# Kernel tuning notes

Measured on AMD Instinct MI355X. Metric: run time of the kernel, lower is better.

## Reference

```python
import jax, jax.numpy as jnp
import numpy as np

EMBED = 256
NUM_DEPTH = 128
NUM_CAMS = 1


def _bilinear_sample(img, x, y):
    # img: [H, W, E]; x, y: [L] pixel coords (align_corners=False, zero padding)
    H, W, _ = img.shape
    x0f = jnp.floor(x); y0f = jnp.floor(y)
    ix0 = x0f.astype(jnp.int32); iy0 = y0f.astype(jnp.int32)
    ix1 = ix0 + 1; iy1 = iy0 + 1
    wx1 = x - x0f; wx0 = 1.0 - wx1
    wy1 = y - y0f; wy0 = 1.0 - wy1

    def g(iy, ix):
        valid = (ix >= 0) & (ix < W) & (iy >= 0) & (iy < H)
        v = img[jnp.clip(iy, 0, H - 1), jnp.clip(ix, 0, W - 1)]  # [L, E]
        return jnp.where(valid[:, None], v, jnp.zeros((), img.dtype))

    return (g(iy0, ix0) * (wy0 * wx0)[:, None] + g(iy0, ix1) * (wy0 * wx1)[:, None]
            + g(iy1, ix0) * (wy1 * wx0)[:, None] + g(iy1, ix1) * (wy1 * wx1)[:, None])


def setup_inputs() -> dict:
    rng = jax.random.key(0)
    ks = jax.random.split(rng, 7)
    H = W = 64
    nv = H * W           # num_value == num_query (forced by output*key broadcast)
    bsv = 1
    return {
        "query": jax.random.normal(ks[0], (bsv, nv, EMBED), jnp.float32),
        "key": jax.random.normal(ks[1], (NUM_CAMS, nv, bsv, EMBED), jnp.float32),
        "value": jax.random.normal(ks[2], (NUM_CAMS, nv, bsv, EMBED), jnp.float32),
        "identity": jax.random.normal(ks[3], (bsv, nv, NUM_DEPTH), jnp.float32),
        "ref_3d": jax.random.uniform(ks[4], (bsv * NUM_CAMS, nv * NUM_DEPTH, 2), jnp.float32),
        "spatial_shapes": jnp.array([[H, W]], jnp.int32),
        "W_attn": jax.random.normal(ks[5], (NUM_CAMS * NUM_DEPTH, EMBED), jnp.float32) * 0.02,
        "b_attn": jax.random.normal(ks[6], (NUM_CAMS * NUM_DEPTH,), jnp.float32) * 0.02,
    }


def reference(query, key, value, identity, ref_3d, spatial_shapes, W_attn, b_attn):
    bsv, num_query, _ = query.shape
    num_cams, num_value, bs, _ = key.shape
    H = int(spatial_shapes[0, 0]); W = int(spatial_shapes[0, 1])

    # key/value rearrange (value flipped over cams dim, a no-op for num_cams=1)
    key_r = jnp.transpose(key, (2, 0, 1, 3)).reshape(bsv, num_value, EMBED)
    val_r = jnp.transpose(value[::-1], (2, 0, 1, 3)).reshape(bsv * num_cams, num_value, EMBED)

    # attention weights: Linear -> softmax over (levels*points)=1 axis (== ones)
    aw = query @ W_attn.T + b_attn                               # [bsv, nq, cams*depth]
    aw = aw.reshape(bsv, num_query, num_cams, NUM_DEPTH, 1, 1)    # heads=1, lv*pt=1
    aw = jax.nn.softmax(aw, axis=-1)
    aw = jnp.transpose(aw.reshape(bsv, num_query, num_cams, NUM_DEPTH, 1, 1, 1),
                       (0, 2, 1, 3, 4, 5, 6))
    aw = aw.reshape(bsv * num_cams, num_query * NUM_DEPTH)        # [B, L]

    # deformable bilinear sampling (single level/head/point)
    grids = 2.0 * ref_3d - 1.0                                   # grid_sample convention
    px = ((grids[..., 0] + 1.0) * W - 1.0) / 2.0                  # [B, L]
    py = ((grids[..., 1] + 1.0) * H - 1.0) / 2.0
    imgs = val_r.reshape(bsv * num_cams, H, W, EMBED)
    sampled = jax.vmap(_bilinear_sample)(imgs, px, py)            # [B, L, E]

    out = sampled * aw[:, :, None]                                # weighted gather
    out = out.reshape(bsv, num_cams, num_query, NUM_DEPTH, EMBED).mean(axis=1)

    # elementwise dot with key features, scaled
    out = jnp.sum(out * key_r[:, :, None, :], axis=-1) / jnp.sqrt(jnp.float32(EMBED))
    return out + identity                                         # [bsv, nq, num_depth]
```

## Files before the change

### kernel.cpp

```cpp
#include <hip/hip_runtime.h>

#define EMBED 256
#define NUM_DEPTH 128
#define CT_STRIDE 136

typedef __attribute__((ext_vector_type(8))) short bf16x8;
typedef __attribute__((ext_vector_type(4))) float f32x4;

__device__ __forceinline__ unsigned short f2b(float f) {
    union { float f; unsigned u; } c; c.f = f;
    unsigned u = c.u;
    u += 0x7fffu + ((u >> 16) & 1u);
    return (unsigned short)(u >> 16);
}
__device__ __forceinline__ float b2f(unsigned short h) {
    union { unsigned u; float f; } c; c.u = ((unsigned)h) << 16;
    return c.f;
}

__global__ __launch_bounds__(256) void cvt_kernel(
    const float4* __restrict__ key, const float4* __restrict__ val,
    ushort4* __restrict__ kb, ushort4* __restrict__ vb, int n4)
{
    int i = blockIdx.x * blockDim.x + threadIdx.x;
    if (i >= n4) return;
    float4 a = key[i];
    float4 b = val[i];
    kb[i] = make_ushort4(f2b(a.x), f2b(a.y), f2b(a.z), f2b(a.w));
    vb[i] = make_ushort4(f2b(b.x), f2b(b.y), f2b(b.z), f2b(b.w));
}

__global__ __launch_bounds__(256) void gemm_nt_bf16(
    const unsigned short* __restrict__ A,
    const unsigned short* __restrict__ B,
    unsigned short* __restrict__ D,
    int N)
{
    __shared__ __align__(16) unsigned short Ct[128 * CT_STRIDE];
    unsigned short* As = Ct;
    unsigned short* Bs = Ct + 128 * 32;

    const int m0 = blockIdx.y * 128;
    const int n0 = blockIdx.x * 128;
    const int tid  = threadIdx.x;
    const int lane = tid & 63;
    const int wave = tid >> 6;
    const int wm = (wave & 1) * 64;
    const int wn = (wave >> 1) * 64;

    f32x4 acc[4][4] = {};

    const int srow = lane >> 2;
    const int scol = (lane & 3) * 8;
    const int k8 = (lane >> 4) * 8;
    const int fm = lane & 15;

    for (int kt = 0; kt < EMBED; kt += 32) {
        #pragma unroll
        for (int t = 0; t < 2; ++t) {
            const int c = wave * 2 + t;
            const int row = c * 16 + srow;
            const unsigned short* ga = A + (size_t)(m0 + row) * EMBED + kt + scol;
            const unsigned short* gb = B + (size_t)(n0 + row) * EMBED + kt + scol;
            __builtin_amdgcn_global_load_lds(
                (const __attribute__((address_space(1))) void*)ga,
                (__attribute__((address_space(3))) void*)(As + c * 512), 16, 0, 0);
            __builtin_amdgcn_global_load_lds(
                (const __attribute__((address_space(1))) void*)gb,
                (__attribute__((address_space(3))) void*)(Bs + c * 512), 16, 0, 0);
        }
        __syncthreads();

        bf16x8 af[4], bfr[4];
        #pragma unroll
        for (int i = 0; i < 4; ++i) {
            af[i]  = *(const bf16x8*)(As + (wm + i * 16 + fm) * 32 + k8);
            bfr[i] = *(const bf16x8*)(Bs + (wn + i * 16 + fm) * 32 + k8);
        }
        #pragma unroll
        for (int i = 0; i < 4; ++i)
            #pragma unroll
            for (int j = 0; j < 4; ++j)
                acc[i][j] = __builtin_amdgcn_mfma_f32_16x16x32_bf16(af[i], bfr[j], acc[i][j], 0, 0, 0);
        __syncthreads();
    }

    const int col = lane & 15;
    const int rbase = (lane >> 4) * 4;
    #pragma unroll
    for (int i = 0; i < 4; ++i)
        #pragma unroll
        for (int j = 0; j < 4; ++j) {
            const int rr = wm + i * 16 + rbase;
            const int cc = wn + j * 16 + col;
            #pragma unroll
            for (int r = 0; r < 4; ++r)
                Ct[(rr + r) * CT_STRIDE + cc] = f2b(acc[i][j][r]);
        }
    __syncthreads();

    #pragma unroll
    for (int it = 0; it < 8; ++it) {
        const int r  = it * 16 + (tid >> 4);
        const int c8 = (tid & 15) * 8;
        const int4 v = *(const int4*)(Ct + r * CT_STRIDE + c8);
        *(int4*)(D + (size_t)(m0 + r) * N + n0 + c8) = v;
    }
}

__global__ __launch_bounds__(256) void gather_kernel(
    const unsigned short* __restrict__ D,
    const float* __restrict__ identity,
    const float* __restrict__ ref3d,
    const int*   __restrict__ spatial,
    float* __restrict__ out, int nv)
{
    __shared__ unsigned short Ds[2 * 4096];

    const int q0 = blockIdx.x * 2;
    const int tid = threadIdx.x;

    const int4* src = (const int4*)(D + (size_t)q0 * nv);
    int4* dst = (int4*)Ds;
    const int nchunk = (2 * nv) / 8;
    for (int i = tid; i < nchunk; i += 256) dst[i] = src[i];
    __syncthreads();

    const int Hs = spatial[0], Ws = spatial[1];
    const int l = q0 * NUM_DEPTH + tid;
    const int qi = tid >> 7;

    const float2 r2 = reinterpret_cast<const float2*>(ref3d)[l];
    const float px = r2.x * (float)Ws - 0.5f;
    const float py = r2.y * (float)Hs - 0.5f;
    const float x0f = floorf(px), y0f = floorf(py);
    const int ix0 = (int)x0f, iy0 = (int)y0f;
    const int ix1 = ix0 + 1,  iy1 = iy0 + 1;
    const float wx1 = px - x0f, wx0 = 1.0f - wx1;
    const float wy1 = py - y0f, wy0 = 1.0f - wy1;
    const bool vx0 = (ix0 >= 0) & (ix0 < Ws);
    const bool vx1 = (ix1 >= 0) & (ix1 < Ws);

    const unsigned short* row = Ds + qi * nv;
    float acc = 0.f;
    if (iy0 >= 0 && iy0 < Hs) {
        if (vx0) acc = fmaf(wy0 * wx0, b2f(row[iy0 * Ws + ix0]), acc);
        if (vx1) acc = fmaf(wy0 * wx1, b2f(row[iy0 * Ws + ix1]), acc);
    }
    if (iy1 >= 0 && iy1 < Hs) {
        if (vx0) acc = fmaf(wy1 * wx0, b2f(row[iy1 * Ws + ix0]), acc);
        if (vx1) acc = fmaf(wy1 * wx1, b2f(row[iy1 * Ws + ix1]), acc);
    }
    out[l] = fmaf(acc, 0.0625f, identity[l]);
}

__global__ __launch_bounds__(256) void uv_direct_kernel(
    const float* __restrict__ key, const float* __restrict__ value,
    const float* __restrict__ identity, const float* __restrict__ ref3d,
    const int* __restrict__ spatial, float* __restrict__ out)
{
    const int q = blockIdx.x;
    const int tid = threadIdx.x;
    const int lane = tid & 63;
    const int wave = tid >> 6;
    const int H = spatial[0], W = spatial[1];
    const int row4 = EMBED / 4;
    const float4 k4 = reinterpret_cast<const float4*>(key + (size_t)q * EMBED)[lane];
    const float4* __restrict__ v4 = reinterpret_cast<const float4*>(value);
    for (int d = wave; d < NUM_DEPTH; d += 4) {
        const int l = q * NUM_DEPTH + d;
        const float rx = ref3d[2 * l], ry = ref3d[2 * l + 1];
        const float px = rx * (float)W - 0.5f, py = ry * (float)H - 0.5f;
        const float x0f = floorf(px), y0f = floorf(py);
        const int ix0 = (int)x0f, iy0 = (int)y0f, ix1 = ix0 + 1, iy1 = iy0 + 1;
        const float wx1 = px - x0f, wx0 = 1.f - wx1, wy1 = py - y0f, wy0 = 1.f - wy1;
        float4 acc = make_float4(0.f, 0.f, 0.f, 0.f);
        #define TAP(IY, IX, WGT) \
            if ((IY) >= 0 && (IY) < H && (IX) >= 0 && (IX) < W) { \
                const float w_ = (WGT); \
                const float4 t = v4[(size_t)((IY) * W + (IX)) * row4 + lane]; \
                acc.x = fmaf(w_, t.x, acc.x); acc.y = fmaf(w_, t.y, acc.y); \
                acc.z = fmaf(w_, t.z, acc.z); acc.w = fmaf(w_, t.w, acc.w); }
        TAP(iy0, ix0, wy0 * wx0) TAP(iy0, ix1, wy0 * wx1)
        TAP(iy1, ix0, wy1 * wx0) TAP(iy1, ix1, wy1 * wx1)
        #undef TAP
        float partial = acc.x * k4.x + acc.y * k4.y + acc.z * k4.z + acc.w * k4.w;
        #pragma unroll
        for (int off = 32; off > 0; off >>= 1) partial += __shfl_xor(partial, off, 64);
        if (lane == 0) out[l] = fmaf(partial, 0.0625f, identity[l]);
    }
}

extern "C" void kernel_launch(void* const* d_in, const int* in_sizes, int n_in,
                              void* d_out, int out_size, void* d_ws, size_t ws_size,
                              hipStream_t stream) {
    const float* key      = (const float*)d_in[1];
    const float* value    = (const float*)d_in[2];
    const float* identity = (const float*)d_in[3];
    const float* ref3d    = (const float*)d_in[4];
    const int*   spatial  = (const int*)d_in[5];
    float* out = (float*)d_out;

    const int nq = in_sizes[3] / NUM_DEPTH;
    const int nv = in_sizes[1] / EMBED;

    const size_t d_bytes  = (size_t)nq * nv * sizeof(unsigned short);
    const size_t kb_bytes = (size_t)nq * EMBED * sizeof(unsigned short);
    const size_t vb_bytes = (size_t)nv * EMBED * sizeof(unsigned short);
    const size_t need = d_bytes + kb_bytes + vb_bytes;

    if (ws_size < need || (nq % 128) || (nv % 128) || nv > 4096 || (nq % 2)) {
        uv_direct_kernel<<<nq, 256, 0, stream>>>(key, value, identity, ref3d, spatial, out);
        return;
    }

    unsigned short* D  = (unsigned short*)d_ws;
    unsigned short* kb = (unsigned short*)((char*)d_ws + d_bytes);
    unsigned short* vb = (unsigned short*)((char*)d_ws + d_bytes + kb_bytes);

    const int n4 = nq * EMBED / 4;
    cvt_kernel<<<(n4 + 255) / 256, 256, 0, stream>>>(
        (const float4*)key, (const float4*)value, (ushort4*)kb, (ushort4*)vb, n4);

    dim3 grid(nv / 128, nq / 128);
    gemm_nt_bf16<<<grid, 256, 0, stream>>>(kb, vb, D, nv);

    gather_kernel<<<nq / 2, 256, 0, stream>>>(D, identity, ref3d, spatial, out, nv);
}
```

Before: 99.56 us.

## Fuse bilinear gather into GEMM epilogue via pre-binned tap lists and atomics

A prep kernel now converts key/value to bf16 and, in the same launch, initialises the output with identity. It also bins every bilinear tap by the value-pixel tile it reads, writing per-(query tile, pixel tile, block) counts and entry lists. The GEMM epilogue then reads each tile's entry list and atomically adds the weighted, scaled dot-product values straight from shared memory into the output. This removes the full nq×nv bf16 intermediate, its write and re-read, and the separate gather launch. In exchange it adds atomics, a workspace for entry lists, and a fixed per-segment capacity that would drop taps if a bin overflows.

```diff
diff --git a/kernel.cpp b/kernel.cpp
--- a/kernel.cpp
+++ b/kernel.cpp
@@ -3,6 +3,8 @@
 #define EMBED 256
 #define NUM_DEPTH 128
 #define CT_STRIDE 136
+#define SEG 128
+#define BPQ 64
 
 typedef __attribute__((ext_vector_type(8))) short bf16x8;
 typedef __attribute__((ext_vector_type(4))) float f32x4;
@@ -18,23 +20,74 @@
     return c.f;
 }
 
-__global__ __launch_bounds__(256) void cvt_kernel(
+__global__ __launch_bounds__(256) void prep_kernel(
     const float4* __restrict__ key, const float4* __restrict__ val,
-    ushort4* __restrict__ kb, ushort4* __restrict__ vb, int n4)
+    ushort4* __restrict__ kb, ushort4* __restrict__ vb, int n4, int cvtBlocks,
+    const float* __restrict__ identity, const float* __restrict__ ref3d,
+    const int* __restrict__ spatial, float* __restrict__ out,
+    unsigned* __restrict__ cnts, unsigned* __restrict__ gent, int NB, int nv)
 {
-    int i = blockIdx.x * blockDim.x + threadIdx.x;
-    if (i >= n4) return;
-    float4 a = key[i];
-    float4 b = val[i];
-    kb[i] = make_ushort4(f2b(a.x), f2b(a.y), f2b(a.z), f2b(a.w));
-    vb[i] = make_ushort4(f2b(b.x), f2b(b.y), f2b(b.z), f2b(b.w));
-}
-
-__global__ __launch_bounds__(256) void gemm_nt_bf16(
+    const int tid = threadIdx.x;
+    if ((int)blockIdx.x < cvtBlocks) {
+        int i = blockIdx.x * 256 + tid;
+        if (i < n4) {
+            float4 a = key[i];
+            float4 b = val[i];
+            kb[i] = make_ushort4(f2b(a.x), f2b(a.y), f2b(a.z), f2b(a.w));
+            vb[i] = make_ushort4(f2b(b.x), f2b(b.y), f2b(b.z), f2b(b.w));
+        }
+        return;
+    }
+
+    __shared__ unsigned cnt[32];
+    if (tid < 32) cnt[tid] = 0;
+    __syncthreads();
+
+    const int bb = blockIdx.x - cvtBlocks;
+    const int l  = bb * 256 + tid;
+    out[l] = identity[l];
+
+    const int Hs = spatial[0], Ws = spatial[1];
+    const float2 r2 = reinterpret_cast<const float2*>(ref3d)[l];
+    const float px = r2.x * (float)Ws - 0.5f;
+    const float py = r2.y * (float)Hs - 0.5f;
+    const float x0f = floorf(px), y0f = floorf(py);
+    const int ix0 = (int)x0f, iy0 = (int)y0f;
+
+    int pbt[4]; unsigned slot[4];
+    #pragma unroll
+    for (int t = 0; t < 4; ++t) {
+        const int ix = ix0 + (t & 1);
+        const int iy = iy0 + (t >> 1);
+        pbt[t] = -1;
+        if (ix >= 0 && ix < Ws && iy >= 0 && iy < Hs) {
+            const int p = iy * Ws + ix;
+            if (p < nv) {
+                pbt[t]  = p >> 7;
+                slot[t] = atomicAdd(&cnt[pbt[t]], 1u);
+            }
+        }
+    }
+    __syncthreads();
+
+    const int qb  = bb >> 6;
+    const int blk = bb & 63;
+    if (tid < NB) cnts[((size_t)qb * NB + tid) * BPQ + blk] = cnt[tid];
+
+    #pragma unroll
+    for (int t = 0; t < 4; ++t)
+        if (pbt[t] >= 0 && slot[t] < SEG)
+            gent[(((size_t)qb * NB + pbt[t]) * BPQ + blk) * SEG + slot[t]] =
+                ((unsigned)l << 2) | (unsigned)t;
+}
+
+__global__ __launch_bounds__(256) void gemm_scatter(
     const unsigned short* __restrict__ A,
     const unsigned short* __restrict__ B,
-    unsigned short* __restrict__ D,
-    int N)
+    const float* __restrict__ ref3d,
+    const int* __restrict__ spatial,
+    float* __restrict__ out,
+    const unsigned* __restrict__ cnts, const unsigned* __restrict__ gent, int NB)
 {
     __shared__ __align__(16) unsigned short Ct[128 * CT_STRIDE];
     unsigned short* As = Ct;
@@ -99,59 +152,30 @@
         }
     __syncthreads();
 
-    #pragma unroll
-    for (int it = 0; it < 8; ++it) {
-        const int r  = it * 16 + (tid >> 4);
-        const int c8 = (tid & 15) * 8;
-        const int4 v = *(const int4*)(Ct + r * CT_STRIDE + c8);
-        *(int4*)(D + (size_t)(m0 + r) * N + n0 + c8) = v;
-    }
-}
-
-__global__ __launch_bounds__(256) void gather_kernel(
-    const unsigned short* __restrict__ D,
-    const float* __restrict__ identity,
-    const float* __restrict__ ref3d,
-    const int*   __restrict__ spatial,
-    float* __restrict__ out, int nv)
-{
-    __shared__ unsigned short Ds[2 * 4096];
-
-    const int q0 = blockIdx.x * 2;
-    const int tid = threadIdx.x;
-
-    const int4* src = (const int4*)(D + (size_t)q0 * nv);
-    int4* dst = (int4*)Ds;
-    const int nchunk = (2 * nv) / 8;
-    for (int i = tid; i < nchunk; i += 256) dst[i] = src[i];
-    __syncthreads();
-
+    const size_t bin = (size_t)blockIdx.y * NB + blockIdx.x;
+    const unsigned* __restrict__ cseg = cnts + bin * BPQ;
+    const unsigned* __restrict__ eseg = gent + bin * BPQ * SEG;
     const int Hs = spatial[0], Ws = spatial[1];
-    const int l = q0 * NUM_DEPTH + tid;
-    const int qi = tid >> 7;
-
-    const float2 r2 = reinterpret_cast<const float2*>(ref3d)[l];
-    const float px = r2.x * (float)Ws - 0.5f;
-    const float py = r2.y * (float)Hs - 0.5f;
-    const float x0f = floorf(px), y0f = floorf(py);
-    const int ix0 = (int)x0f, iy0 = (int)y0f;
-    const int ix1 = ix0 + 1,  iy1 = iy0 + 1;
-    const float wx1 = px - x0f, wx0 = 1.0f - wx1;
-    const float wy1 = py - y0f, wy0 = 1.0f - wy1;
-    const bool vx0 = (ix0 >= 0) & (ix0 < Ws);
-    const bool vx1 = (ix1 >= 0) & (ix1 < Ws);
-
-    const unsigned short* row = Ds + qi * nv;
-    float acc = 0.f;
-    if (iy0 >= 0 && iy0 < Hs) {
-        if (vx0) acc = fmaf(wy0 * wx0, b2f(row[iy0 * Ws + ix0]), acc);
-        if (vx1) acc = fmaf(wy0 * wx1, b2f(row[iy0 * Ws + ix1]), acc);
-    }
-    if (iy1 >= 0 && iy1 < Hs) {
-        if (vx0) acc = fmaf(wy1 * wx0, b2f(row[iy1 * Ws + ix0]), acc);
-        if (vx1) acc = fmaf(wy1 * wx1, b2f(row[iy1 * Ws + ix1]), acc);
-    }
-    out[l] = fmaf(acc, 0.0625f, identity[l]);
+
+    const int seg = tid & 63;
+    const unsigned c = min(cseg[seg], (unsigned)SEG);
+    for (unsigned i = (unsigned)(tid >> 6); i < c; i += 4) {
+        const unsigned e = eseg[seg * SEG + i];
+        const int l = (int)(e >> 2);
+        const int t = (int)(e & 3u);
+        const float2 r2 = reinterpret_cast<const float2*>(ref3d)[l];
+        const float px = r2.x * (float)Ws - 0.5f;
+        const float py = r2.y * (float)Hs - 0.5f;
+        const float x0f = floorf(px), y0f = floorf(py);
+        const float fx = px - x0f, fy = py - y0f;
+        const float wx = (t & 1) ? fx : 1.0f - fx;
+        const float wy = (t & 2) ? fy : 1.0f - fy;
+        const int ix = (int)x0f + (t & 1);
+        const int iy = (int)y0f + ((t >> 1) & 1);
+        const int p = iy * Ws + ix;
+        const float v = b2f(Ct[((l >> 7) & 127) * CT_STRIDE + (p & 127)]);
+        atomicAdd(out + l, wx * wy * v * 0.0625f);
+    }
 }
 
 __global__ __launch_bounds__(256) void uv_direct_kernel(
@@ -204,26 +228,30 @@
     const int nq = in_sizes[3] / NUM_DEPTH;
     const int nv = in_sizes[1] / EMBED;
 
-    const size_t d_bytes  = (size_t)nq * nv * sizeof(unsigned short);
-    const size_t kb_bytes = (size_t)nq * EMBED * sizeof(unsigned short);
-    const size_t vb_bytes = (size_t)nv * EMBED * sizeof(unsigned short);
-    const size_t need = d_bytes + kb_bytes + vb_bytes;
-
-    if (ws_size < need || (nq % 128) || (nv % 128) || nv > 4096 || (nq % 2)) {
+    const int MB = nq >> 7, NB = nv >> 7;
+    const size_t kb_bytes  = (size_t)nq * EMBED * sizeof(unsigned short);
+    const size_t vb_bytes  = (size_t)nv * EMBED * sizeof(unsigned short);
+    const size_t cnt_bytes = (size_t)MB * NB * BPQ * sizeof(unsigned);
+    const size_t ent_bytes = (size_t)MB * NB * BPQ * SEG * sizeof(unsigned);
+    const size_t need = kb_bytes + vb_bytes + cnt_bytes + ent_bytes;
+
+    if (ws_size < need || (nq % 128) || (nv % 128) || nv > 4096 || nq != nv) {
         uv_direct_kernel<<<nq, 256, 0, stream>>>(key, value, identity, ref3d, spatial, out);
         return;
     }
 
-    unsigned short* D  = (unsigned short*)d_ws;
-    unsigned short* kb = (unsigned short*)((char*)d_ws + d_bytes);
-    unsigned short* vb = (unsigned short*)((char*)d_ws + d_bytes + kb_bytes);
+    unsigned short* kb = (unsigned short*)d_ws;
+    unsigned short* vb = (unsigned short*)((char*)d_ws + kb_bytes);
+    unsigned* cnts = (unsigned*)((char*)d_ws + kb_bytes + vb_bytes);
+    unsigned* gent = cnts + (size_t)MB * NB * BPQ;
 
     const int n4 = nq * EMBED / 4;
-    cvt_kernel<<<(n4 + 255) / 256, 256, 0, stream>>>(
-        (const float4*)key, (const float4*)value, (ushort4*)kb, (ushort4*)vb, n4);
-
-    dim3 grid(nv / 128, nq / 128);
-    gemm_nt_bf16<<<grid, 256, 0, stream>>>(kb, vb, D, nv);
-
-    gather_kernel<<<nq / 2, 256, 0, stream>>>(D, identity, ref3d, spatial, out, nv);
-}
+    const int cvtBlocks = (n4 + 255) / 256;
+    const int binBlocks = nq * NUM_DEPTH / 256;
+    prep_kernel<<<cvtBlocks + binBlocks, 256, 0, stream>>>(
+        (const float4*)key, (const float4*)value, (ushort4*)kb, (ushort4*)vb,
+        n4, cvtBlocks, identity, ref3d, spatial, out, cnts, gent, NB, nv);
+
+    dim3 grid(NB, MB);
+    gemm_scatter<<<grid, 256, 0, stream>>>(kb, vb, ref3d, spatial, out, cnts, gent, NB);
+}
```

After: 204.6 us. 2.05x slower.

## Shrink GEMM tile to 128x64 with XCD-aware block remap and direct stores

Applied to the files above, without the earlier changes.

Halves the N tile of the bf16 GEMM to 64, so the 4096x4096 output uses twice as many workgroups and per-block LDS and register use drops (launch bounds now ask for 6 blocks per CU). Workgroup ids are remapped so consecutive tiles sharing A rows land on the same XCD, which should improve L2 reuse. The LDS staging epilogue is removed and results are written straight to global with 2-byte scattered stores, which saves LDS traffic and a barrier but gives up wide coalesced writes. It also adds an nq==nv guard on the fast path.

```diff
diff --git a/kernel.cpp b/kernel.cpp
--- a/kernel.cpp
+++ b/kernel.cpp
@@ -2,7 +2,6 @@
 
 #define EMBED 256
 #define NUM_DEPTH 128
-#define CT_STRIDE 136
 
 typedef __attribute__((ext_vector_type(8))) short bf16x8;
 typedef __attribute__((ext_vector_type(4))) float f32x4;
@@ -30,25 +29,30 @@
     vb[i] = make_ushort4(f2b(b.x), f2b(b.y), f2b(b.z), f2b(b.w));
 }
 
-__global__ __launch_bounds__(256) void gemm_nt_bf16(
+__global__ __launch_bounds__(256, 6) void gemm_nt_bf16(
     const unsigned short* __restrict__ A,
     const unsigned short* __restrict__ B,
     unsigned short* __restrict__ D,
-    int N)
-{
-    __shared__ __align__(16) unsigned short Ct[128 * CT_STRIDE];
-    unsigned short* As = Ct;
-    unsigned short* Bs = Ct + 128 * 32;
-
-    const int m0 = blockIdx.y * 128;
-    const int n0 = blockIdx.x * 128;
+    int N, int NBl)
+{
+    __shared__ __align__(16) unsigned short As[128 * 32];
+    __shared__ __align__(16) unsigned short Bs[64 * 32];
+
+    const int nwg = gridDim.x;
+    const int xcd = blockIdx.x & 7;
+    const int off = blockIdx.x >> 3;
+    const int qch = nwg >> 3, rch = nwg & 7;
+    const int wg = (xcd < rch ? xcd * (qch + 1) : rch * (qch + 1) + (xcd - rch) * qch) + off;
+
+    const int m0 = (wg / NBl) * 128;
+    const int n0 = (wg % NBl) * 64;
     const int tid  = threadIdx.x;
     const int lane = tid & 63;
     const int wave = tid >> 6;
     const int wm = (wave & 1) * 64;
-    const int wn = (wave >> 1) * 64;
-
-    f32x4 acc[4][4] = {};
+    const int wn = (wave >> 1) * 32;
+
+    f32x4 acc[4][2] = {};
 
     const int srow = lane >> 2;
     const int scol = (lane & 3) * 8;
@@ -61,26 +65,31 @@
             const int c = wave * 2 + t;
             const int row = c * 16 + srow;
             const unsigned short* ga = A + (size_t)(m0 + row) * EMBED + kt + scol;
-            const unsigned short* gb = B + (size_t)(n0 + row) * EMBED + kt + scol;
             __builtin_amdgcn_global_load_lds(
                 (const __attribute__((address_space(1))) void*)ga,
                 (__attribute__((address_space(3))) void*)(As + c * 512), 16, 0, 0);
+        }
+        {
+            const int c = wave;
+            const int row = c * 16 + srow;
+            const unsigned short* gb = B + (size_t)(n0 + row) * EMBED + kt + scol;
             __builtin_amdgcn_global_load_lds(
                 (const __attribute__((address_space(1))) void*)gb,
                 (__attribute__((address_space(3))) void*)(Bs + c * 512), 16, 0, 0);
         }
         __syncthreads();
 
-        bf16x8 af[4], bfr[4];
-        #pragma unroll
-        for (int i = 0; i < 4; ++i) {
+        bf16x8 af[4], bfr[2];
+        #pragma unroll
+        for (int i = 0; i < 4; ++i)
             af[i]  = *(const bf16x8*)(As + (wm + i * 16 + fm) * 32 + k8);
-            bfr[i] = *(const bf16x8*)(Bs + (wn + i * 16 + fm) * 32 + k8);
-        }
+        #pragma unroll
+        for (int j = 0; j < 2; ++j)
+            bfr[j] = *(const bf16x8*)(Bs + (wn + j * 16 + fm) * 32 + k8);
         #pragma unroll
         for (int i = 0; i < 4; ++i)
             #pragma unroll
-            for (int j = 0; j < 4; ++j)
+            for (int j = 0; j < 2; ++j)
                 acc[i][j] = __builtin_amdgcn_mfma_f32_16x16x32_bf16(af[i], bfr[j], acc[i][j], 0, 0, 0);
         __syncthreads();
     }
@@ -90,22 +99,12 @@
     #pragma unroll
     for (int i = 0; i < 4; ++i)
         #pragma unroll
-        for (int j = 0; j < 4; ++j) {
-            const int rr = wm + i * 16 + rbase;
-            const int cc = wn + j * 16 + col;
+        for (int j = 0; j < 2; ++j) {
+            const int cc = n0 + wn + j * 16 + col;
             #pragma unroll
             for (int r = 0; r < 4; ++r)
-                Ct[(rr + r) * CT_STRIDE + cc] = f2b(acc[i][j][r]);
+                D[(size_t)(m0 + wm + i * 16 + rbase + r) * N + cc] = f2b(acc[i][j][r]);
         }
-    __syncthreads();
-
-    #pragma unroll
-    for (int it = 0; it < 8; ++it) {
-        const int r  = it * 16 + (tid >> 4);
-        const int c8 = (tid & 15) * 8;
-        const int4 v = *(const int4*)(Ct + r * CT_STRIDE + c8);
-        *(int4*)(D + (size_t)(m0 + r) * N + n0 + c8) = v;
-    }
 }
 
 __global__ __launch_bounds__(256) void gather_kernel(
@@ -209,7 +208,7 @@
     const size_t vb_bytes = (size_t)nv * EMBED * sizeof(unsigned short);
     const size_t need = d_bytes + kb_bytes + vb_bytes;
 
-    if (ws_size < need || (nq % 128) || (nv % 128) || nv > 4096 || (nq % 2)) {
+    if (ws_size < need || (nq % 128) || (nv % 128) || nv > 4096 || (nq % 2) || nq != nv) {
         uv_direct_kernel<<<nq, 256, 0, stream>>>(key, value, identity, ref3d, spatial, out);
         return;
     }
@@ -222,8 +221,9 @@
     cvt_kernel<<<(n4 + 255) / 256, 256, 0, stream>>>(
         (const float4*)key, (const float4*)value, (ushort4*)kb, (ushort4*)vb, n4);
 
-    dim3 grid(nv / 128, nq / 128);
-    gemm_nt_bf16<<<grid, 256, 0, stream>>>(kb, vb, D, nv);
+    const int NBl = nv / 64;
+    const int nwg = (nq / 128) * NBl;
+    gemm_nt_bf16<<<nwg, 256, 0, stream>>>(kb, vb, D, nv, NBl);
 
     gather_kernel<<<nq / 2, 256, 0, stream>>>(D, identity, ref3d, spatial, out, nv);
 }
```

Result: slower. 103.2 us (+3.7%).
